# Kernel tuning notes

Hardware: AMD Instinct MI355X
Metric: run time of the kernel (lower is better)

The kernel has to match this reference:

```python
import jax, jax.numpy as jnp
import numpy as np

EMBEDDING_DIM = 256
N_PITCHES = 128
N_VELOCITIES = 128
VOCAB_SIZE = 50257
N_CHORDS = 24
N_BEATS = 16
N_MELS = 128
N_GENRES = 10
N_TEMPOS = 10
N_KEYS = 12
N_MODES = 2
D_IN = EMBEDDING_DIM + N_PITCHES + N_VELOCITIES + VOCAB_SIZE + N_CHORDS + N_BEATS + N_MELS  # 50937
D_LYR = D_IN - EMBEDDING_DIM - N_PITCHES - N_VELOCITIES  # 50425
LENGTH = 16
T = LENGTH * N_PITCHES  # 2048 steps
EMB_VOCAB = N_GENRES + N_TEMPOS + N_KEYS + N_MODES + 1  # 35


def setup_inputs() -> dict:
    key = jax.random.key(0)
    ks = jax.random.split(key, 12)
    s = 1.0 / np.sqrt(D_IN).astype(np.float32)
    return dict(
        genre=jax.random.randint(ks[0], (1,), 0, N_GENRES, dtype=jnp.int64 if jax.config.jax_enable_x64 else jnp.int32),
        tempo=jax.random.randint(ks[1], (1,), 0, N_TEMPOS),
        key_sig=jax.random.randint(ks[2], (1,), 0, N_KEYS),
        length=LENGTH,
        melody_tensor=jax.random.normal(ks[3], (T, N_PITCHES + N_VELOCITIES), jnp.float32),
        lyrics_tensor=jax.random.normal(ks[4], (T, D_LYR), jnp.float32),
        emb=jax.random.normal(ks[5], (EMB_VOCAB, EMBEDDING_DIM), jnp.float32) * 0.02,
        conv_w=jax.random.normal(ks[6], (1, 1, 3, 3), jnp.float32) * (1.0 / 3.0),
        conv_b=jnp.zeros((1,), jnp.float32),
        w_chord=jax.random.normal(ks[7], (D_IN, N_CHORDS), jnp.float32) * s,
        b_chord=jnp.zeros((N_CHORDS,), jnp.float32),
        w_beat=jax.random.normal(ks[8], (D_IN, N_BEATS), jnp.float32) * s,
        b_beat=jnp.zeros((N_BEATS,), jnp.float32),
        w_mel=jax.random.normal(ks[9], (D_IN, N_MELS), jnp.float32) * s,
        b_mel=jnp.zeros((N_MELS,), jnp.float32),
    )


def reference(genre, tempo, key_sig, length, melody_tensor, lyrics_tensor,
              emb, conv_w, conv_b, w_chord, b_chord, w_beat, b_beat, w_mel, b_mel):
    # context ids: genre/tempo/key offset into the shared embedding table; last slot for the length token
    ids = jnp.concatenate([
        genre,
        tempo + N_GENRES,
        key_sig + N_GENRES + N_TEMPOS,
        jnp.array([EMB_VOCAB - 1], dtype=genre.dtype),
    ])
    ctx = emb[ids].sum(axis=0)  # [EMBEDDING_DIM]
    t = melody_tensor.shape[0]  # length * N_PITCHES steps, all batched
    # per-step 50937-dim feature vector: [context | melody pitch+vel | lyrics/state]
    x = jnp.concatenate([
        jnp.broadcast_to(ctx, (t, EMBEDDING_DIM)),
        melody_tensor,
        lyrics_tensor,
    ], axis=1)  # [T, D_IN]
    # 3x3 SAME conv on each step viewed as a 1x1xD_IN image (single in/out channel)
    xc = jax.lax.conv_general_dilated(
        x[:, None, None, :], conv_w,
        window_strides=(1, 1), padding=((1, 1), (1, 1)),
        dimension_numbers=('NCHW', 'OIHW', 'NCHW'))
    xc = xc[:, 0, 0, :] + conv_b[0]  # [T, D_IN]
    # three large-K linear heads, concatenated along features
    out = jnp.concatenate([
        xc @ w_chord + b_chord,
        xc @ w_beat + b_beat,
        xc @ w_mel + b_mel,
    ], axis=1)  # [T, N_CHORDS+N_BEATS+N_MELS] = [T, 168]
    return out
```

## Files before the change

### kernel.cpp

```cpp
#include <hip/hip_runtime.h>

#define D_IN_   50937
#define D_LYR_  50425
#define T_      2048
#define NCH     24
#define NBE     16
#define NME     128
#define NOUT    168
#define NPAD    192
#define KROWS   50688
#define KSPLIT  16
#define TOTSTEP 792
#define PARTN   (2048*168)

typedef __attribute__((ext_vector_type(8))) short short8;
typedef __attribute__((ext_vector_type(4))) float f32x4;
typedef float f32x4u __attribute__((ext_vector_type(4), aligned(4)));
typedef __attribute__((ext_vector_type(2))) unsigned int u32x2;

static __device__ __forceinline__ unsigned short f2bf(float f) {
    unsigned int u = __float_as_uint(f);
    u += 0x7FFF + ((u >> 16) & 1);
    return (unsigned short)(u >> 16);
}
static __device__ __forceinline__ unsigned int pack2(float x, float y) {
    return (unsigned int)f2bf(x) | ((unsigned int)f2bf(y) << 16);
}

static __device__ __forceinline__ float wsrc(const float* wc, const float* wb,
                                             const float* wm, int d, int n) {
    if (n < NCH)        return wc[d * NCH + n];
    if (n < NCH + NBE)  return wb[d * NBE + (n - NCH)];
    if (n < NOUT)       return wm[(long)d * NME + (n - NCH - NBE)];
    return 0.f;
}
static __device__ __forceinline__ f32x4 wsrc4(const float* wc, const float* wb,
                                              const float* wm, int d, int nq) {
    int n0 = nq * 4;
    if (n0 < 24)  return *(const f32x4*)(wc + d * 24 + n0);
    if (n0 < 40)  return *(const f32x4*)(wb + d * 16 + (n0 - 24));
    if (n0 < 168) return *(const f32x4*)(wm + (long)d * 128 + (n0 - 40));
    f32x4 z = {0.f, 0.f, 0.f, 0.f};
    return z;
}

__global__ void k_ctx(const int* genre, const int* tempo, const int* keysig,
                      const float* emb, float* ctx) {
    int d = threadIdx.x;
    int g = genre[0], t = tempo[0], k = keysig[0];
    ctx[d] = emb[g * 256 + d] + emb[(10 + t) * 256 + d] +
             emb[(20 + k) * 256 + d] + emb[34 * 256 + d];
}

__global__ __launch_bounds__(256) void k_fold(const float* wc, const float* wb,
                                              const float* wm_, const float* conv_w,
                                              unsigned short* wbt) {
    __shared__ unsigned short tile[64 * 196];
    float cw0 = conv_w[3], cw1 = conv_w[4], cw2 = conv_w[5];
    int r0 = blockIdx.x * 64;
    int tid = threadIdx.x;
    for (int i = 0; i < 12; ++i) {
        int idx = tid + i * 256;
        int dl = idx / 48, nq = idx % 48;
        int r = r0 + dl;
        f32x4 v = {0.f, 0.f, 0.f, 0.f};
        if (r < 50681) {
            int d = 256 + r;
            f32x4 w0 = wsrc4(wc, wb, wm_, d, nq);
            f32x4 wn1 = wsrc4(wc, wb, wm_, d - 1, nq);
            v = cw1 * w0 + cw2 * wn1;
            if (d + 1 < D_IN_) v += cw0 * wsrc4(wc, wb, wm_, d + 1, nq);
        }
        u32x2 p; p.x = pack2(v.x, v.y); p.y = pack2(v.z, v.w);
        *(u32x2*)&tile[dl * 196 + nq * 4] = p;
    }
    __syncthreads();
    for (int i = 0; i < 6; ++i) {
        int idx = tid + i * 256;
        int n = idx >> 3, ch = idx & 7;
        short8 o;
        for (int j = 0; j < 8; ++j) o[j] = (short)tile[(ch * 8 + j) * 196 + n];
        *(short8*)(wbt + (long)n * KROWS + r0 + ch * 8) = o;
    }
}

__global__ void k_cvec(const float* wc, const float* wb, const float* wm_,
                       const float* conv_w, const float* conv_b,
                       const float* bc, const float* bb, const float* bm_,
                       const float* ctx, float* C) {
    int j = blockIdx.x;
    int lane = threadIdx.x;
    float cw0 = conv_w[3], cw1 = conv_w[4], cw2 = conv_w[5];
    float s = 0.f;
    for (int d = lane; d < 256; d += 64) {
        float wp = cw1 * wsrc(wc, wb, wm_, d, j) + cw0 * wsrc(wc, wb, wm_, d + 1, j);
        if (d > 0) wp += cw2 * wsrc(wc, wb, wm_, d - 1, j);
        s += ctx[d] * wp;
    }
    float cb = conv_b[0];
    if (cb != 0.f) {
        float cs = 0.f;
        for (int d = lane; d < D_IN_; d += 64) cs += wsrc(wc, wb, wm_, d, j);
        s += cb * cs;
    }
    for (int off = 32; off; off >>= 1) s += __shfl_down(s, off);
    if (lane == 0) {
        float b = (j < NCH) ? bc[j] : (j < NCH + NBE) ? bb[j - NCH] : bm_[j - NCH - NBE];
        C[j] = s + b;
    }
}

static __device__ __forceinline__ f32x4 loadArow(const float* mel, const float* lyr,
                                                 int t, int r) {
    if (r < 256) return *(const f32x4u*)(mel + t * 256 + r);
    int c = r - 256;
    if (c + 3 < D_LYR_) return *(const f32x4u*)(lyr + (long)t * D_LYR_ + c);
    f32x4 v;
    for (int j = 0; j < 4; ++j)
        v[j] = (c + j < D_LYR_) ? lyr[(long)t * D_LYR_ + c + j] : 0.f;
    return v;
}

__global__ __launch_bounds__(512, 4) void k_gemm(const float* mel, const float* lyr,
                                                 const unsigned short* wbt,
                                                 float* partial) {
    __shared__ unsigned short As[2 * 64 * 64];
    __shared__ unsigned short Bs[2 * 192 * 64];
    int blk = blockIdx.x;
    int ks = ((blk & 7) << 1) | ((blk >> 3) & 1);
    int bm = blk >> 4;
    int tid = threadIdx.x, lane = tid & 63, wv = tid >> 6;
    int wm = wv & 1, wn = wv >> 1;
    f32x4 zero4 = {0.f, 0.f, 0.f, 0.f};
    f32x4 acc[2][3];
    for (int mi = 0; mi < 2; ++mi)
        for (int ni = 0; ni < 3; ++ni) acc[mi][ni] = zero4;

    int start = ks * 49 + (ks < 8 ? ks : 8);
    int cnt = 49 + (ks < 8 ? 1 : 0);

    int f4 = tid & 15, rowl = tid >> 4;
    int bn = tid >> 3, bch = tid & 7;

    {
        int r0 = start * 64;
        f32x4 a0 = loadArow(mel, lyr, bm * 64 + rowl, r0 + f4 * 4);
        f32x4 a1 = loadArow(mel, lyr, bm * 64 + rowl + 32, r0 + f4 * 4);
        short8 brg[3];
        for (int i = 0; i < 3; ++i) {
            int n = bn + i * 64;
            brg[i] = *(const short8*)(wbt + (long)n * KROWS + r0 + bch * 8);
        }
        int rb0 = rowl, rb1 = rowl + 32;
        u32x2 p0; p0.x = pack2(a0.x, a0.y); p0.y = pack2(a0.z, a0.w);
        u32x2 p1; p1.x = pack2(a1.x, a1.y); p1.y = pack2(a1.z, a1.w);
        *(u32x2*)((char*)As + rb0 * 128 + ((f4 * 8) ^ ((rb0 & 7) << 4))) = p0;
        *(u32x2*)((char*)As + rb1 * 128 + ((f4 * 8) ^ ((rb1 & 7) << 4))) = p1;
        for (int i = 0; i < 3; ++i) {
            int n = bn + i * 64;
            *(short8*)((char*)Bs + n * 128 + ((bch * 16) ^ ((n & 7) << 4))) = brg[i];
        }
    }
    __syncthreads();

    for (int t = 0; t < cnt; ++t) {
        const char* Ac = (const char*)As + (t & 1) * 8192;
        const char* Bc = (const char*)Bs + (t & 1) * 24576;
        char* An = (char*)As + ((t & 1) ^ 1) * 8192;
        char* Bn = (char*)Bs + ((t & 1) ^ 1) * 24576;
        bool pf = (t + 1 < cnt);
        f32x4 a0, a1; short8 brg[3];
        if (pf) {
            int r0 = (start + t + 1) * 64;
            a0 = loadArow(mel, lyr, bm * 64 + rowl, r0 + f4 * 4);
            a1 = loadArow(mel, lyr, bm * 64 + rowl + 32, r0 + f4 * 4);
            for (int i = 0; i < 3; ++i) {
                int n = bn + i * 64;
                brg[i] = *(const short8*)(wbt + (long)n * KROWS + r0 + bch * 8);
            }
        }
        for (int kk = 0; kk < 2; ++kk) {
            short8 af[2], bfr[3];
            for (int mi = 0; mi < 2; ++mi) {
                int row = wm * 32 + mi * 16 + (lane & 15);
                int byte = row * 128 +
                           (((kk * 64) + ((lane >> 4) * 16)) ^ ((row & 7) << 4));
                af[mi] = *(const short8*)(Ac + byte);
            }
            for (int ni = 0; ni < 3; ++ni) {
                int n = wn * 48 + ni * 16 + (lane & 15);
                int byte = n * 128 +
                           (((kk * 64) + ((lane >> 4) * 16)) ^ ((n & 7) << 4));
                bfr[ni] = *(const short8*)(Bc + byte);
            }
            for (int mi = 0; mi < 2; ++mi)
                for (int ni = 0; ni < 3; ++ni)
                    acc[mi][ni] = __builtin_amdgcn_mfma_f32_16x16x32_bf16(
                        af[mi], bfr[ni], acc[mi][ni], 0, 0, 0);
        }
        if (pf) {
            int rb0 = rowl, rb1 = rowl + 32;
            u32x2 p0; p0.x = pack2(a0.x, a0.y); p0.y = pack2(a0.z, a0.w);
            u32x2 p1; p1.x = pack2(a1.x, a1.y); p1.y = pack2(a1.z, a1.w);
            *(u32x2*)(An + rb0 * 128 + ((f4 * 8) ^ ((rb0 & 7) << 4))) = p0;
            *(u32x2*)(An + rb1 * 128 + ((f4 * 8) ^ ((rb1 & 7) << 4))) = p1;
            for (int i = 0; i < 3; ++i) {
                int n = bn + i * 64;
                *(short8*)(Bn + n * 128 + ((bch * 16) ^ ((n & 7) << 4))) = brg[i];
            }
        }
        __syncthreads();
    }

    float* pbase = partial + (long)ks * PARTN;
    for (int mi = 0; mi < 2; ++mi) {
        int rbase = bm * 64 + wm * 32 + mi * 16 + ((lane >> 4) * 4);
        for (int ni = 0; ni < 3; ++ni) {
            int col = wn * 48 + ni * 16 + (lane & 15);
            if (col < NOUT) {
                for (int q = 0; q < 4; ++q)
                    pbase[(long)(rbase + q) * NOUT + col] = acc[mi][ni][q];
            }
        }
    }
}

__global__ void k_reduce(const float* partial, const float* C, float* out) {
    int idx = blockIdx.x * 256 + threadIdx.x;
    if (idx >= PARTN) return;
    int j = idx % NOUT;
    float s = C[j];
    for (int ks = 0; ks < KSPLIT; ++ks) s += partial[(long)ks * PARTN + idx];
    out[idx] = s;
}

extern "C" void kernel_launch(void* const* d_in, const int* in_sizes, int n_in,
                              void* d_out, int out_size, void* d_ws, size_t ws_size,
                              hipStream_t stream) {
    const int*   genre   = (const int*)d_in[0];
    const int*   tempo   = (const int*)d_in[1];
    const int*   keysig  = (const int*)d_in[2];
    const float* mel     = (const float*)d_in[4];
    const float* lyr     = (const float*)d_in[5];
    const float* emb     = (const float*)d_in[6];
    const float* conv_w  = (const float*)d_in[7];
    const float* conv_b  = (const float*)d_in[8];
    const float* w_chord = (const float*)d_in[9];
    const float* b_chord = (const float*)d_in[10];
    const float* w_beat  = (const float*)d_in[11];
    const float* b_beat  = (const float*)d_in[12];
    const float* w_mel   = (const float*)d_in[13];
    const float* b_mel   = (const float*)d_in[14];

    char* ws = (char*)d_ws;
    unsigned short* wbt = (unsigned short*)ws;
    float* ctx     = (float*)(ws + 19464192);
    float* Cvec    = (float*)(ws + 19464192 + 1024);
    float* partial = (float*)(ws + 19466240);
    float* out     = (float*)d_out;

    hipLaunchKernelGGL(k_ctx, dim3(1), dim3(256), 0, stream,
                       genre, tempo, keysig, emb, ctx);
    hipLaunchKernelGGL(k_fold, dim3(TOTSTEP), dim3(256), 0, stream,
                       w_chord, w_beat, w_mel, conv_w, wbt);
    hipLaunchKernelGGL(k_cvec, dim3(168), dim3(64), 0, stream,
                       w_chord, w_beat, w_mel, conv_w, conv_b,
                       b_chord, b_beat, b_mel, ctx, Cvec);
    hipLaunchKernelGGL(k_gemm, dim3(512), dim3(512), 0, stream,
                       mel, lyr, wbt, partial);
    hipLaunchKernelGGL(k_reduce, dim3(1344), dim3(256), 0, stream,
                       partial, Cvec, out);
}
```

Before: 180.9 us.

## Load A fragments directly to registers and stage B via global_load_lds

The GEMM kernel stops staging the activation tile through shared memory. Each wave now loads its A fragment straight from global into registers and converts it to bf16 at MFMA time. The weight tile is copied global-to-LDS with the async global_load_lds builtin, using a pre-swizzled source address, and the wave tiling becomes 4x2 with six accumulators per wave. The context-embedding kernel is folded into k_cvec and the reduce kernel is vectorised to float4, removing one launch and LDS write traffic at the cost of uncoalesced, redundant A reads from global.

```diff
diff --git a/kernel.cpp b/kernel.cpp
--- a/kernel.cpp
+++ b/kernel.cpp
@@ -2,7 +2,6 @@
 
 #define D_IN_   50937
 #define D_LYR_  50425
-#define T_      2048
 #define NCH     24
 #define NBE     16
 #define NME     128
@@ -17,6 +16,8 @@
 typedef __attribute__((ext_vector_type(4))) float f32x4;
 typedef float f32x4u __attribute__((ext_vector_type(4), aligned(4)));
 typedef __attribute__((ext_vector_type(2))) unsigned int u32x2;
+typedef __attribute__((address_space(3))) unsigned int lds_u32;
+typedef const __attribute__((address_space(1))) unsigned int glob_u32;
 
 static __device__ __forceinline__ unsigned short f2bf(float f) {
     unsigned int u = __float_as_uint(f);
@@ -42,14 +43,6 @@
     if (n0 < 168) return *(const f32x4*)(wm + (long)d * 128 + (n0 - 40));
     f32x4 z = {0.f, 0.f, 0.f, 0.f};
     return z;
-}
-
-__global__ void k_ctx(const int* genre, const int* tempo, const int* keysig,
-                      const float* emb, float* ctx) {
-    int d = threadIdx.x;
-    int g = genre[0], t = tempo[0], k = keysig[0];
-    ctx[d] = emb[g * 256 + d] + emb[(10 + t) * 256 + d] +
-             emb[(20 + k) * 256 + d] + emb[34 * 256 + d];
 }
 
 __global__ __launch_bounds__(256) void k_fold(const float* wc, const float* wb,
@@ -84,18 +77,22 @@
     }
 }
 
-__global__ void k_cvec(const float* wc, const float* wb, const float* wm_,
+__global__ void k_cvec(const int* genre, const int* tempo, const int* keysig,
+                       const float* emb,
+                       const float* wc, const float* wb, const float* wm_,
                        const float* conv_w, const float* conv_b,
-                       const float* bc, const float* bb, const float* bm_,
-                       const float* ctx, float* C) {
+                       const float* bc, const float* bb, const float* bm_, float* C) {
     int j = blockIdx.x;
     int lane = threadIdx.x;
+    int g = genre[0], tt = tempo[0], kk = keysig[0];
     float cw0 = conv_w[3], cw1 = conv_w[4], cw2 = conv_w[5];
     float s = 0.f;
     for (int d = lane; d < 256; d += 64) {
+        float cx = emb[g * 256 + d] + emb[(10 + tt) * 256 + d] +
+                   emb[(20 + kk) * 256 + d] + emb[34 * 256 + d];
         float wp = cw1 * wsrc(wc, wb, wm_, d, j) + cw0 * wsrc(wc, wb, wm_, d + 1, j);
         if (d > 0) wp += cw2 * wsrc(wc, wb, wm_, d - 1, j);
-        s += ctx[d] * wp;
+        s += cx * wp;
     }
     float cb = conv_b[0];
     if (cb != 0.f) {
@@ -110,128 +107,124 @@
     }
 }
 
-static __device__ __forceinline__ f32x4 loadArow(const float* mel, const float* lyr,
-                                                 int t, int r) {
-    if (r < 256) return *(const f32x4u*)(mel + t * 256 + r);
-    int c = r - 256;
-    if (c + 3 < D_LYR_) return *(const f32x4u*)(lyr + (long)t * D_LYR_ + c);
-    f32x4 v;
-    for (int j = 0; j < 4; ++j)
-        v[j] = (c + j < D_LYR_) ? lyr[(long)t * D_LYR_ + c + j] : 0.f;
-    return v;
-}
-
 __global__ __launch_bounds__(512, 4) void k_gemm(const float* mel, const float* lyr,
                                                  const unsigned short* wbt,
                                                  float* partial) {
-    __shared__ unsigned short As[2 * 64 * 64];
-    __shared__ unsigned short Bs[2 * 192 * 64];
-    int blk = blockIdx.x;
-    int ks = ((blk & 7) << 1) | ((blk >> 3) & 1);
-    int bm = blk >> 4;
-    int tid = threadIdx.x, lane = tid & 63, wv = tid >> 6;
-    int wm = wv & 1, wn = wv >> 1;
-    f32x4 zero4 = {0.f, 0.f, 0.f, 0.f};
-    f32x4 acc[2][3];
-    for (int mi = 0; mi < 2; ++mi)
-        for (int ni = 0; ni < 3; ++ni) acc[mi][ni] = zero4;
-
-    int start = ks * 49 + (ks < 8 ? ks : 8);
-    int cnt = 49 + (ks < 8 ? 1 : 0);
-
-    int f4 = tid & 15, rowl = tid >> 4;
-    int bn = tid >> 3, bch = tid & 7;
-
-    {
-        int r0 = start * 64;
-        f32x4 a0 = loadArow(mel, lyr, bm * 64 + rowl, r0 + f4 * 4);
-        f32x4 a1 = loadArow(mel, lyr, bm * 64 + rowl + 32, r0 + f4 * 4);
-        short8 brg[3];
-        for (int i = 0; i < 3; ++i) {
-            int n = bn + i * 64;
-            brg[i] = *(const short8*)(wbt + (long)n * KROWS + r0 + bch * 8);
-        }
-        int rb0 = rowl, rb1 = rowl + 32;
-        u32x2 p0; p0.x = pack2(a0.x, a0.y); p0.y = pack2(a0.z, a0.w);
-        u32x2 p1; p1.x = pack2(a1.x, a1.y); p1.y = pack2(a1.z, a1.w);
-        *(u32x2*)((char*)As + rb0 * 128 + ((f4 * 8) ^ ((rb0 & 7) << 4))) = p0;
-        *(u32x2*)((char*)As + rb1 * 128 + ((f4 * 8) ^ ((rb1 & 7) << 4))) = p1;
-        for (int i = 0; i < 3; ++i) {
-            int n = bn + i * 64;
-            *(short8*)((char*)Bs + n * 128 + ((bch * 16) ^ ((n & 7) << 4))) = brg[i];
-        }
-    }
+    __shared__ unsigned short Bs[2 * NPAD * 64];
+    const int blk = blockIdx.x;
+    const int ks = ((blk & 7) << 1) | ((blk >> 3) & 1);
+    const int bm = blk >> 4;
+    const int tid = threadIdx.x, lane = tid & 63, wv = tid >> 6;
+    const int wm = wv >> 1, wn = wv & 1;
+    const int start = ks * 49 + (ks < 8 ? ks : 8);
+    const int cnt = 49 + (ks < 8 ? 1 : 0);
+    const int arow = bm * 64 + wm * 16 + (lane & 15);
+    const int kq = (lane >> 4) * 8;
+    const int l15 = lane & 15;
+    const int bnl = lane >> 3, bcs = lane & 7;
+
+    f32x4 acc[6];
+    for (int i = 0; i < 6; ++i) acc[i] = (f32x4){0.f, 0.f, 0.f, 0.f};
+
+    auto stageB = [&](int t, int buf) {
+        int r0 = (start + t) * 64;
+        #pragma unroll
+        for (int j = 0; j < 3; ++j) {
+            int n0 = wv * 24 + j * 8;
+            int n = n0 + bnl;
+            const unsigned short* gp =
+                wbt + (long)n * KROWS + r0 + ((bcs ^ (n & 7)) * 8);
+            __builtin_amdgcn_global_load_lds((glob_u32*)gp,
+                                             (lds_u32*)(Bs + buf * (NPAD * 64) + n0 * 64),
+                                             16, 0, 0);
+        }
+    };
+
+    auto loadA = [&](int t, f32x4u* dst) {
+        int gt = start + t;
+        int r0 = gt * 64;
+        #pragma unroll
+        for (int kk2 = 0; kk2 < 2; ++kk2) {
+            int r = r0 + kk2 * 32 + kq;
+            if (r < 256) {
+                dst[kk2 * 2]     = *(const f32x4u*)(mel + arow * 256 + r);
+                dst[kk2 * 2 + 1] = *(const f32x4u*)(mel + arow * 256 + r + 4);
+            } else {
+                long b = (long)arow * D_LYR_ + (r - 256);
+                if (gt != TOTSTEP - 1) {
+                    dst[kk2 * 2]     = *(const f32x4u*)(lyr + b);
+                    dst[kk2 * 2 + 1] = *(const f32x4u*)(lyr + b + 4);
+                } else {
+                    int c = r - 256;
+                    f32x4 v0, v1;
+                    for (int q = 0; q < 4; ++q) {
+                        v0[q] = (c + q     < D_LYR_) ? lyr[b + q]     : 0.f;
+                        v1[q] = (c + 4 + q < D_LYR_) ? lyr[b + 4 + q] : 0.f;
+                    }
+                    dst[kk2 * 2] = v0; dst[kk2 * 2 + 1] = v1;
+                }
+            }
+        }
+    };
+
+    auto computeT = [&](const f32x4u* areg, int bufc) {
+        const char* Bb = (const char*)(Bs + bufc * (NPAD * 64));
+        #pragma unroll
+        for (int kk2 = 0; kk2 < 2; ++kk2) {
+            f32x4 a0 = areg[kk2 * 2], a1 = areg[kk2 * 2 + 1];
+            short8 af;
+            af[0] = (short)f2bf(a0.x); af[1] = (short)f2bf(a0.y);
+            af[2] = (short)f2bf(a0.z); af[3] = (short)f2bf(a0.w);
+            af[4] = (short)f2bf(a1.x); af[5] = (short)f2bf(a1.y);
+            af[6] = (short)f2bf(a1.z); af[7] = (short)f2bf(a1.w);
+            #pragma unroll
+            for (int ni = 0; ni < 6; ++ni) {
+                int n = wn * 96 + ni * 16 + l15;
+                int slot = (kk2 * 4 + (lane >> 4)) ^ (n & 7);
+                short8 bf = *(const short8*)(Bb + n * 128 + slot * 16);
+                acc[ni] = __builtin_amdgcn_mfma_f32_16x16x32_bf16(af, bf, acc[ni], 0, 0, 0);
+            }
+        }
+    };
+
+    f32x4u aA[4], aB[4];
+    loadA(0, aA);
+    stageB(0, 0);
     __syncthreads();
-
-    for (int t = 0; t < cnt; ++t) {
-        const char* Ac = (const char*)As + (t & 1) * 8192;
-        const char* Bc = (const char*)Bs + (t & 1) * 24576;
-        char* An = (char*)As + ((t & 1) ^ 1) * 8192;
-        char* Bn = (char*)Bs + ((t & 1) ^ 1) * 24576;
-        bool pf = (t + 1 < cnt);
-        f32x4 a0, a1; short8 brg[3];
-        if (pf) {
-            int r0 = (start + t + 1) * 64;
-            a0 = loadArow(mel, lyr, bm * 64 + rowl, r0 + f4 * 4);
-            a1 = loadArow(mel, lyr, bm * 64 + rowl + 32, r0 + f4 * 4);
-            for (int i = 0; i < 3; ++i) {
-                int n = bn + i * 64;
-                brg[i] = *(const short8*)(wbt + (long)n * KROWS + r0 + bch * 8);
-            }
-        }
-        for (int kk = 0; kk < 2; ++kk) {
-            short8 af[2], bfr[3];
-            for (int mi = 0; mi < 2; ++mi) {
-                int row = wm * 32 + mi * 16 + (lane & 15);
-                int byte = row * 128 +
-                           (((kk * 64) + ((lane >> 4) * 16)) ^ ((row & 7) << 4));
-                af[mi] = *(const short8*)(Ac + byte);
-            }
-            for (int ni = 0; ni < 3; ++ni) {
-                int n = wn * 48 + ni * 16 + (lane & 15);
-                int byte = n * 128 +
-                           (((kk * 64) + ((lane >> 4) * 16)) ^ ((n & 7) << 4));
-                bfr[ni] = *(const short8*)(Bc + byte);
-            }
-            for (int mi = 0; mi < 2; ++mi)
-                for (int ni = 0; ni < 3; ++ni)
-                    acc[mi][ni] = __builtin_amdgcn_mfma_f32_16x16x32_bf16(
-                        af[mi], bfr[ni], acc[mi][ni], 0, 0, 0);
-        }
-        if (pf) {
-            int rb0 = rowl, rb1 = rowl + 32;
-            u32x2 p0; p0.x = pack2(a0.x, a0.y); p0.y = pack2(a0.z, a0.w);
-            u32x2 p1; p1.x = pack2(a1.x, a1.y); p1.y = pack2(a1.z, a1.w);
-            *(u32x2*)(An + rb0 * 128 + ((f4 * 8) ^ ((rb0 & 7) << 4))) = p0;
-            *(u32x2*)(An + rb1 * 128 + ((f4 * 8) ^ ((rb1 & 7) << 4))) = p1;
-            for (int i = 0; i < 3; ++i) {
-                int n = bn + i * 64;
-                *(short8*)(Bn + n * 128 + ((bch * 16) ^ ((n & 7) << 4))) = brg[i];
-            }
-        }
+    int t = 0;
+    while (true) {
+        if (t + 1 < cnt) { loadA(t + 1, aB); stageB(t + 1, 1); }
+        computeT(aA, 0);
         __syncthreads();
+        if (++t >= cnt) break;
+        if (t + 1 < cnt) { loadA(t + 1, aA); stageB(t + 1, 0); }
+        computeT(aB, 1);
+        __syncthreads();
+        if (++t >= cnt) break;
     }
 
     float* pbase = partial + (long)ks * PARTN;
-    for (int mi = 0; mi < 2; ++mi) {
-        int rbase = bm * 64 + wm * 32 + mi * 16 + ((lane >> 4) * 4);
-        for (int ni = 0; ni < 3; ++ni) {
-            int col = wn * 48 + ni * 16 + (lane & 15);
-            if (col < NOUT) {
-                for (int q = 0; q < 4; ++q)
-                    pbase[(long)(rbase + q) * NOUT + col] = acc[mi][ni][q];
-            }
+    int rb = bm * 64 + wm * 16 + ((lane >> 4) * 4);
+    #pragma unroll
+    for (int ni = 0; ni < 6; ++ni) {
+        int col = wn * 96 + ni * 16 + l15;
+        if (col < NOUT) {
+            #pragma unroll
+            for (int q = 0; q < 4; ++q)
+                pbase[(long)(rb + q) * NOUT + col] = acc[ni][q];
         }
     }
 }
 
 __global__ void k_reduce(const float* partial, const float* C, float* out) {
     int idx = blockIdx.x * 256 + threadIdx.x;
-    if (idx >= PARTN) return;
-    int j = idx % NOUT;
-    float s = C[j];
-    for (int ks = 0; ks < KSPLIT; ++ks) s += partial[(long)ks * PARTN + idx];
-    out[idx] = s;
+    if (idx >= PARTN / 4) return;
+    int base = idx * 4;
+    f32x4 s;
+    for (int q = 0; q < 4; ++q) s[q] = C[(base + q) % NOUT];
+    for (int ks = 0; ks < KSPLIT; ++ks)
+        s += *(const f32x4*)(partial + (long)ks * PARTN + base);
+    *(f32x4*)(out + base) = s;
 }
 
 extern "C" void kernel_launch(void* const* d_in, const int* in_sizes, int n_in,
@@ -254,20 +247,18 @@
 
     char* ws = (char*)d_ws;
     unsigned short* wbt = (unsigned short*)ws;
-    float* ctx     = (float*)(ws + 19464192);
-    float* Cvec    = (float*)(ws + 19464192 + 1024);
+    float* Cvec    = (float*)(ws + 19464192);
     float* partial = (float*)(ws + 19466240);
     float* out     = (float*)d_out;
 
-    hipLaunchKernelGGL(k_ctx, dim3(1), dim3(256), 0, stream,
-                       genre, tempo, keysig, emb, ctx);
     hipLaunchKernelGGL(k_fold, dim3(TOTSTEP), dim3(256), 0, stream,
                        w_chord, w_beat, w_mel, conv_w, wbt);
-    hipLaunchKernelGGL(k_cvec, dim3(168), dim3(64), 0, stream,
+    hipLaunchKernelGGL(k_cvec, dim3(NOUT), dim3(64), 0, stream,
+                       genre, tempo, keysig, emb,
                        w_chord, w_beat, w_mel, conv_w, conv_b,
-                       b_chord, b_beat, b_mel, ctx, Cvec);
+                       b_chord, b_beat, b_mel, Cvec);
     hipLaunchKernelGGL(k_gemm, dim3(512), dim3(512), 0, stream,
                        mel, lyr, wbt, partial);
-    hipLaunchKernelGGL(k_reduce, dim3(1344), dim3(256), 0, stream,
+    hipLaunchKernelGGL(k_reduce, dim3((PARTN / 4 + 255) / 256), dim3(256), 0, stream,
                        partial, Cvec, out);
 }
```

New measurement: 227.8 us. 26.0% more time.
